# Kernel optimization log

Measured on AMD Instinct MI355X. Metric: run time of the kernel, lower is better.

Reference implementation:

```python
import jax, jax.numpy as jnp
import numpy as np

DIM = 512
CODEBOOK_SIZE = 8192
CODEBOOK_DIM = 13  # log2(8192)
CODEBOOK_SCALE = 1.0
DIVERSITY_GAMMA = 1.0
COMMIT_W = 0.25
ENTROPY_W = 0.1
EPS = 1e-5


def make_codebook():
    mask = 2 ** jnp.arange(CODEBOOK_DIM - 1, -1, -1)  # [13]
    codes = jnp.arange(CODEBOOK_SIZE)
    bits = ((codes[:, None] & mask) != 0).astype(jnp.float32)
    return bits * 2.0 * CODEBOOK_SCALE - CODEBOOK_SCALE  # [8192, 13]


def setup_inputs() -> dict:
    key = jax.random.key(0)
    k1, k2, k3, k4, k5 = jax.random.split(key, 5)
    x = jax.random.normal(k1, (4, 2048, DIM), dtype=jnp.float32)
    w_in = jax.random.normal(k2, (DIM, CODEBOOK_DIM), dtype=jnp.float32) * (DIM ** -0.5)
    b_in = jax.random.normal(k3, (CODEBOOK_DIM,), dtype=jnp.float32) * 0.01
    w_out = jax.random.normal(k4, (CODEBOOK_DIM, DIM), dtype=jnp.float32) * (CODEBOOK_DIM ** -0.5)
    b_out = jax.random.normal(k5, (DIM,), dtype=jnp.float32) * 0.01
    return {"x": x, "w_in": w_in, "b_in": b_in, "w_out": w_out, "b_out": b_out,
            "codebook": make_codebook()}


def reference(x, w_in, b_in, w_out, b_out, codebook):
    # project_in: [b, n, dim] -> [b, n, cd]
    h = jnp.einsum('bnd,dc->bnc', x, w_in) + b_in
    original_input = h

    # sign quantization
    quantized = jnp.where(h > 0, CODEBOOK_SCALE, -CODEBOOK_SCALE).astype(h.dtype)
    bit_mask = 2 ** jnp.arange(CODEBOOK_DIM - 1, -1, -1, dtype=jnp.int32)
    indices = jnp.sum((quantized > 0).astype(jnp.int32) * bit_mask, axis=-1)  # [b, n]

    # straight-through estimator (training branch)
    xq = h + jax.lax.stop_gradient(quantized - h)

    # entropy aux loss: affinity = -distance = 2 * <orig, codebook>
    logits = 2.0 * jnp.einsum('bnc,kc->bnk', original_input, codebook)  # [b, n, K]
    probs = jax.nn.softmax(logits, axis=-1)
    log_probs = jax.nn.log_softmax(logits + EPS, axis=-1)
    per_sample_entropy = -jnp.mean(jnp.sum(probs * log_probs, axis=-1))
    avg_probs = jnp.mean(probs.reshape(-1, CODEBOOK_SIZE), axis=0)
    codebook_entropy = -jnp.sum(avg_probs * jnp.log(avg_probs + EPS))
    entropy_aux_loss = 1.0 * per_sample_entropy - DIVERSITY_GAMMA * codebook_entropy

    # commitment loss
    commit_loss = jnp.mean((original_input - jax.lax.stop_gradient(quantized)) ** 2)

    # project_out
    out = jnp.einsum('bnc,cd->bnd', xq, w_out) + b_out

    aux_loss = entropy_aux_loss * ENTROPY_W + commit_loss * COMMIT_W
    return out, indices, aux_loss
```

## Files before the change

### kernel.cpp

```cpp
#include <hip/hip_runtime.h>
#include <math.h>

#define NTOK 8192
#define DIMV 512
#define CD 13
#define KSZ 8192
#define NPARTS 512
#define TPB 16

#define C_BYTES  ((size_t)NPARTS * KSZ * 4)
#define PC_OFF   C_BYTES
#define E_OFF    (PC_OFF + 4096)
#define CNT_OFF  (E_OFF + 1024)

__global__ __launch_bounds__(512) void ka_fused(const float* __restrict__ x,
                                                const float* __restrict__ w_in,
                                                const float* __restrict__ b_in,
                                                const float* __restrict__ w_out,
                                                const float* __restrict__ b_out,
                                                float* __restrict__ ws_C,
                                                float* __restrict__ ws_pc,
                                                unsigned int* __restrict__ ws_cnt,
                                                float* __restrict__ outv,
                                                float* __restrict__ out_ind) {
  __shared__ __align__(16) float s_winT[CD * DIMV];
  __shared__ float sh[TPB][CD];
  __shared__ __align__(16) float sA[TPB][4][16];
  __shared__ __align__(16) float sB[TPB][128];
  __shared__ float s_cm[TPB], s_pe[TPB];
  int t = threadIdx.x;

  if (blockIdx.x == 0 && t == 0) *ws_cnt = 0u;

  {
    int d = t;
#pragma unroll
    for (int c = 0; c < CD; ++c) s_winT[c * DIMV + d] = w_in[d * CD + c];
  }
  __syncthreads();

  int lane = t & 63;
  int wave = t >> 6;
  int l31 = lane & 31;
  int grp = lane >> 5;
  int tok = wave * 2 + grp;
  int n = blockIdx.x * TPB + tok;

  const float4* x4 = (const float4*)(x + (size_t)n * DIMV);

  float facc[CD];
#pragma unroll
  for (int c = 0; c < CD; ++c) facc[c] = 0.f;
#pragma unroll
  for (int j = 0; j < 4; ++j) {
    float4 xv = x4[l31 + j * 32];
    int dbase = (l31 + j * 32) * 4;
#pragma unroll
    for (int c = 0; c < CD; ++c) {
      const float4 wv = *(const float4*)&s_winT[c * DIMV + dbase];
      facc[c] += xv.x * wv.x + xv.y * wv.y + xv.z * wv.z + xv.w * wv.w;
    }
  }
  double acc[CD];
#pragma unroll
  for (int c = 0; c < CD; ++c) {
    double a = (double)facc[c];
    a += __shfl_xor(a, 1, 64);
    a += __shfl_xor(a, 2, 64);
    a += __shfl_xor(a, 4, 64);
    a += __shfl_xor(a, 8, 64);
    a += __shfl_xor(a, 16, 64);
    acc[c] = a + (double)b_in[c];
  }

  int idx = 0;
#pragma unroll
  for (int c = 0; c < CD; ++c) idx |= (acc[c] > 0.0 ? 1 : 0) << (12 - c);
  if (l31 == 0) out_ind[n] = (float)idx;

  float hv = 0.f;
#pragma unroll
  for (int c = 0; c < CD; ++c) if (l31 == c) hv = (float)acc[c];
  float cm = 0.f, pe = 0.f;
  if (l31 < CD) {
    sh[tok][l31] = hv;
    float a = fabsf(hv);
    float d1 = a - 1.f;
    cm = d1 * d1;
    float z = 4.f * a;
    float e = expf(-z);
    pe = log1pf(e) + z * e / (1.f + e);
  }
  cm += __shfl_xor(cm, 1, 64); pe += __shfl_xor(pe, 1, 64);
  cm += __shfl_xor(cm, 2, 64); pe += __shfl_xor(pe, 2, 64);
  cm += __shfl_xor(cm, 4, 64); pe += __shfl_xor(pe, 4, 64);
  cm += __shfl_xor(cm, 8, 64); pe += __shfl_xor(pe, 8, 64);
  cm += __shfl_xor(cm, 16, 64); pe += __shfl_xor(pe, 16, 64);
  if (l31 == 0) { s_cm[tok] = cm; s_pe[tok] = pe; }

  int dpos = lane * 4;
  int id2[2];
  id2[0] = __shfl(idx, 0, 64);
  id2[1] = __shfl(idx, 32, 64);
  float4 o[2][2];
  {
    float4 bo0 = *(const float4*)(b_out + dpos);
    float4 bo1 = *(const float4*)(b_out + dpos + 256);
#pragma unroll
    for (int tt = 0; tt < 2; ++tt) { o[tt][0] = bo0; o[tt][1] = bo1; }
  }
#pragma unroll
  for (int c = 0; c < CD; ++c) {
    const float4 w0 = *(const float4*)&w_out[c * DIMV + dpos];
    const float4 w1 = *(const float4*)&w_out[c * DIMV + dpos + 256];
#pragma unroll
    for (int tt = 0; tt < 2; ++tt) {
      float sgn = ((id2[tt] >> (12 - c)) & 1) ? 1.f : -1.f;
      o[tt][0].x = fmaf(sgn, w0.x, o[tt][0].x);
      o[tt][0].y = fmaf(sgn, w0.y, o[tt][0].y);
      o[tt][0].z = fmaf(sgn, w0.z, o[tt][0].z);
      o[tt][0].w = fmaf(sgn, w0.w, o[tt][0].w);
      o[tt][1].x = fmaf(sgn, w1.x, o[tt][1].x);
      o[tt][1].y = fmaf(sgn, w1.y, o[tt][1].y);
      o[tt][1].z = fmaf(sgn, w1.z, o[tt][1].z);
      o[tt][1].w = fmaf(sgn, w1.w, o[tt][1].w);
    }
  }
  int n0 = blockIdx.x * TPB + wave * 2;
#pragma unroll
  for (int tt = 0; tt < 2; ++tt) {
    float4* dst = (float4*)(outv + (size_t)(n0 + tt) * DIMV);
    dst[lane] = o[tt][0];
    dst[lane + 64] = o[tt][1];
  }

  __syncthreads();
  if (t == 0) {
    float C = 0.f, P = 0.f;
#pragma unroll
    for (int i = 0; i < TPB; ++i) { C += s_cm[i]; P += s_pe[i]; }
    ws_pc[blockIdx.x * 2] = C;
    ws_pc[blockIdx.x * 2 + 1] = P;
  }

#pragma unroll
  for (int mm = 0; mm < 2; ++mm) {
    int m = wave * 2 + mm;
    float p[CD], q[CD];
#pragma unroll
    for (int c = 0; c < CD; ++c) {
      float hvv = sh[m][c];
      float e = expf(-4.f * hvv);
      float r = 1.f / (1.f + e);
      p[c] = r;
      q[c] = e * r;
    }
    float A = ((lane >> 5) & 1) ? p[0] : q[0];
    A *= ((lane >> 4) & 1) ? p[1] : q[1];
    A *= ((lane >> 3) & 1) ? p[2] : q[2];
    A *= ((lane >> 2) & 1) ? p[3] : q[3];
    A *= ((lane >> 1) & 1) ? p[4] : q[4];
    A *= (lane & 1) ? p[5] : q[5];
    sA[m][lane & 3][lane >> 2] = A;
    float Bb = ((lane >> 5) & 1) ? p[7] : q[7];
    Bb *= ((lane >> 4) & 1) ? p[8] : q[8];
    Bb *= ((lane >> 3) & 1) ? p[9] : q[9];
    Bb *= ((lane >> 2) & 1) ? p[10] : q[10];
    Bb *= ((lane >> 1) & 1) ? p[11] : q[11];
    Bb *= (lane & 1) ? p[12] : q[12];
    sB[m][lane] = q[6] * Bb;
    sB[m][64 + lane] = p[6] * Bb;
  }
  __syncthreads();

  int c2 = t >> 7;
  int klo = t & 127;
  float acc2[16];
#pragma unroll
  for (int j = 0; j < 16; ++j) acc2[j] = 0.f;
  for (int m = 0; m < TPB; ++m) {
    float Bv = sB[m][klo];
    const float4* A4 = (const float4*)&sA[m][c2][0];
#pragma unroll
    for (int jj = 0; jj < 4; ++jj) {
      float4 a = A4[jj];
      acc2[jj * 4 + 0] = fmaf(a.x, Bv, acc2[jj * 4 + 0]);
      acc2[jj * 4 + 1] = fmaf(a.y, Bv, acc2[jj * 4 + 1]);
      acc2[jj * 4 + 2] = fmaf(a.z, Bv, acc2[jj * 4 + 2]);
      acc2[jj * 4 + 3] = fmaf(a.w, Bv, acc2[jj * 4 + 3]);
    }
  }
  float* dst = ws_C + (size_t)blockIdx.x * KSZ;
#pragma unroll
  for (int j = 0; j < 16; ++j) dst[t + 512 * j] = acc2[j];
}

__global__ __launch_bounds__(256) void kb_final(const float* __restrict__ ws_C,
                                                const float* __restrict__ ws_pc,
                                                float* __restrict__ ws_e,
                                                unsigned int* __restrict__ ws_cnt,
                                                float* __restrict__ d_aux) {
  __shared__ float red[256];
  __shared__ int s_last;
  int t = threadIdx.x;
  int sl = t & 31, pg = t >> 5;
  int s = blockIdx.x * 32 + sl;
  float a0 = 0.f, a1 = 0.f, a2 = 0.f, a3 = 0.f;
  for (int i = 0; i < 64; i += 4) {
    a0 += ws_C[(size_t)(pg + 8 * (i + 0)) * KSZ + s];
    a1 += ws_C[(size_t)(pg + 8 * (i + 1)) * KSZ + s];
    a2 += ws_C[(size_t)(pg + 8 * (i + 2)) * KSZ + s];
    a3 += ws_C[(size_t)(pg + 8 * (i + 3)) * KSZ + s];
  }
  red[t] = (a0 + a1) + (a2 + a3);
  __syncthreads();
  float contrib = 0.f;
  if (t < 32) {
    float v = red[t];
#pragma unroll
    for (int j = 1; j < 8; ++j) v += red[t + 32 * j];
    float avg = v * (1.f / (float)NTOK);
    contrib = -avg * logf(avg + 1e-5f);
  }
  if (t < 64) {
    contrib += __shfl_xor(contrib, 1, 64);
    contrib += __shfl_xor(contrib, 2, 64);
    contrib += __shfl_xor(contrib, 4, 64);
    contrib += __shfl_xor(contrib, 8, 64);
    contrib += __shfl_xor(contrib, 16, 64);
    if (t == 0) ws_e[blockIdx.x] = contrib;
  }
  if (t == 0) {
    __threadfence();
    unsigned int old = atomicAdd(ws_cnt, 1u);
    s_last = (old == 255u) ? 1 : 0;
  }
  __syncthreads();
  if (s_last) {
    __threadfence();
    __shared__ float rc[256], rp[256], re[256];
    float cm2 = 0.f, pe2 = 0.f;
    for (int i = t; i < 512; i += 256) {
      cm2 += ws_pc[2 * i];
      pe2 += ws_pc[2 * i + 1];
    }
    rc[t] = cm2; rp[t] = pe2; re[t] = ws_e[t];
    __syncthreads();
    if (t < 64) {
      float C = rc[t] + rc[t + 64] + rc[t + 128] + rc[t + 192];
      float P = rp[t] + rp[t + 64] + rp[t + 128] + rp[t + 192];
      float E = re[t] + re[t + 64] + re[t + 128] + re[t + 192];
      C += __shfl_xor(C, 1, 64); P += __shfl_xor(P, 1, 64); E += __shfl_xor(E, 1, 64);
      C += __shfl_xor(C, 2, 64); P += __shfl_xor(P, 2, 64); E += __shfl_xor(E, 2, 64);
      C += __shfl_xor(C, 4, 64); P += __shfl_xor(P, 4, 64); E += __shfl_xor(E, 4, 64);
      C += __shfl_xor(C, 8, 64); P += __shfl_xor(P, 8, 64); E += __shfl_xor(E, 8, 64);
      C += __shfl_xor(C, 16, 64); P += __shfl_xor(P, 16, 64); E += __shfl_xor(E, 16, 64);
      C += __shfl_xor(C, 32, 64); P += __shfl_xor(P, 32, 64); E += __shfl_xor(E, 32, 64);
      if (t == 0) {
        float commit = C * (1.f / (float)(NTOK * CD));
        float psE = P * (1.f / (float)NTOK);
        d_aux[0] = 0.1f * (psE - E) + 0.25f * commit;
      }
    }
  }
}

extern "C" void kernel_launch(void* const* d_in, const int* in_sizes, int n_in,
                              void* d_out, int out_size, void* d_ws, size_t ws_size,
                              hipStream_t stream) {
  const float* x     = (const float*)d_in[0];
  const float* w_in  = (const float*)d_in[1];
  const float* b_in  = (const float*)d_in[2];
  const float* w_out = (const float*)d_in[3];
  const float* b_out = (const float*)d_in[4];

  float* outv = (float*)d_out;
  float* ind  = outv + (size_t)NTOK * DIMV;
  float* aux  = ind + NTOK;

  float*        ws_C   = (float*)d_ws;
  float*        ws_pc  = (float*)((char*)d_ws + PC_OFF);
  float*        ws_e   = (float*)((char*)d_ws + E_OFF);
  unsigned int* ws_cnt = (unsigned int*)((char*)d_ws + CNT_OFF);

  ka_fused<<<NPARTS, 512, 0, stream>>>(x, w_in, b_in, w_out, b_out,
                                       ws_C, ws_pc, ws_cnt, outv, ind);
  kb_final<<<256, 256, 0, stream>>>(ws_C, ws_pc, ws_e, ws_cnt, aux);
}
```

Measured before the change: 43.22 us.

## Halve block size, read w_in from global, and register-tile the codebook outer product

The fused kernel now runs 256 threads per block instead of 512, so each wave handles four tokens instead of two. The shared-memory transpose of w_in is dropped: each lane loads its 52 w_in values straight from global (L2-cached) into registers. The per-block A⊗B outer product is re-tiled so each thread computes an 8x4 register tile with float4 LDS reads and float4 stores, replacing scalar strided stores. This removes the w_in staging and its barrier and improves store vectorisation, at the cost of more registers per thread and fewer threads per block.

```diff
diff --git a/kernel.cpp b/kernel.cpp
--- a/kernel.cpp
+++ b/kernel.cpp
@@ -13,7 +13,7 @@
 #define E_OFF    (PC_OFF + 4096)
 #define CNT_OFF  (E_OFF + 1024)
 
-__global__ __launch_bounds__(512) void ka_fused(const float* __restrict__ x,
+__global__ __launch_bounds__(256) void ka_fused(const float* __restrict__ x,
                                                 const float* __restrict__ w_in,
                                                 const float* __restrict__ b_in,
                                                 const float* __restrict__ w_out,
@@ -23,118 +23,126 @@
                                                 unsigned int* __restrict__ ws_cnt,
                                                 float* __restrict__ outv,
                                                 float* __restrict__ out_ind) {
-  __shared__ __align__(16) float s_winT[CD * DIMV];
   __shared__ float sh[TPB][CD];
-  __shared__ __align__(16) float sA[TPB][4][16];
+  __shared__ __align__(16) float sA[TPB][64];
   __shared__ __align__(16) float sB[TPB][128];
   __shared__ float s_cm[TPB], s_pe[TPB];
   int t = threadIdx.x;
 
   if (blockIdx.x == 0 && t == 0) *ws_cnt = 0u;
-
-  {
-    int d = t;
-#pragma unroll
-    for (int c = 0; c < CD; ++c) s_winT[c * DIMV + d] = w_in[d * CD + c];
-  }
-  __syncthreads();
 
   int lane = t & 63;
   int wave = t >> 6;
   int l31 = lane & 31;
   int grp = lane >> 5;
-  int tok = wave * 2 + grp;
-  int n = blockIdx.x * TPB + tok;
-
-  const float4* x4 = (const float4*)(x + (size_t)n * DIMV);
-
-  float facc[CD];
-#pragma unroll
-  for (int c = 0; c < CD; ++c) facc[c] = 0.f;
-#pragma unroll
-  for (int j = 0; j < 4; ++j) {
-    float4 xv = x4[l31 + j * 32];
-    int dbase = (l31 + j * 32) * 4;
+  int tok = wave * 4 + grp * 2;
+  const float4* wf4 = (const float4*)w_in;
+
+#pragma unroll
+  for (int tt = 0; tt < 2; ++tt) {
+    int tk = tok + tt;
+    int n = blockIdx.x * TPB + tk;
+    const float4* x4 = (const float4*)(x + (size_t)n * DIMV);
+
+    float facc[CD];
+#pragma unroll
+    for (int c = 0; c < CD; ++c) facc[c] = 0.f;
+#pragma unroll
+    for (int j = 0; j < 4; ++j) {
+      int dbase = (l31 + j * 32) * 4;
+      float4 xv = x4[l31 + j * 32];
+      float wreg[52];
+      const float4* wsrc = wf4 + (size_t)(dbase * CD) / 4;
+#pragma unroll
+      for (int k = 0; k < 13; ++k) *(float4*)&wreg[k * 4] = wsrc[k];
+#pragma unroll
+      for (int c = 0; c < CD; ++c) {
+        facc[c] += xv.x * wreg[c] + xv.y * wreg[13 + c] +
+                   xv.z * wreg[26 + c] + xv.w * wreg[39 + c];
+      }
+    }
+    double acc[CD];
 #pragma unroll
     for (int c = 0; c < CD; ++c) {
-      const float4 wv = *(const float4*)&s_winT[c * DIMV + dbase];
-      facc[c] += xv.x * wv.x + xv.y * wv.y + xv.z * wv.z + xv.w * wv.w;
-    }
-  }
-  double acc[CD];
-#pragma unroll
-  for (int c = 0; c < CD; ++c) {
-    double a = (double)facc[c];
-    a += __shfl_xor(a, 1, 64);
-    a += __shfl_xor(a, 2, 64);
-    a += __shfl_xor(a, 4, 64);
-    a += __shfl_xor(a, 8, 64);
-    a += __shfl_xor(a, 16, 64);
-    acc[c] = a + (double)b_in[c];
-  }
-
-  int idx = 0;
-#pragma unroll
-  for (int c = 0; c < CD; ++c) idx |= (acc[c] > 0.0 ? 1 : 0) << (12 - c);
-  if (l31 == 0) out_ind[n] = (float)idx;
-
-  float hv = 0.f;
-#pragma unroll
-  for (int c = 0; c < CD; ++c) if (l31 == c) hv = (float)acc[c];
-  float cm = 0.f, pe = 0.f;
-  if (l31 < CD) {
-    sh[tok][l31] = hv;
-    float a = fabsf(hv);
-    float d1 = a - 1.f;
-    cm = d1 * d1;
-    float z = 4.f * a;
-    float e = expf(-z);
-    pe = log1pf(e) + z * e / (1.f + e);
-  }
-  cm += __shfl_xor(cm, 1, 64); pe += __shfl_xor(pe, 1, 64);
-  cm += __shfl_xor(cm, 2, 64); pe += __shfl_xor(pe, 2, 64);
-  cm += __shfl_xor(cm, 4, 64); pe += __shfl_xor(pe, 4, 64);
-  cm += __shfl_xor(cm, 8, 64); pe += __shfl_xor(pe, 8, 64);
-  cm += __shfl_xor(cm, 16, 64); pe += __shfl_xor(pe, 16, 64);
-  if (l31 == 0) { s_cm[tok] = cm; s_pe[tok] = pe; }
-
-  int dpos = lane * 4;
-  int id2[2];
-  id2[0] = __shfl(idx, 0, 64);
-  id2[1] = __shfl(idx, 32, 64);
-  float4 o[2][2];
+      double a = (double)facc[c];
+      a += __shfl_xor(a, 1, 64);
+      a += __shfl_xor(a, 2, 64);
+      a += __shfl_xor(a, 4, 64);
+      a += __shfl_xor(a, 8, 64);
+      a += __shfl_xor(a, 16, 64);
+      acc[c] = a + (double)b_in[c];
+    }
+
+    int idx = 0;
+#pragma unroll
+    for (int c = 0; c < CD; ++c) idx |= (acc[c] > 0.0 ? 1 : 0) << (12 - c);
+    if (l31 == 0) out_ind[n] = (float)idx;
+
+    float hv = 0.f;
+#pragma unroll
+    for (int c = 0; c < CD; ++c) if (l31 == c) hv = (float)acc[c];
+    float cm = 0.f, pe = 0.f;
+    if (l31 < CD) {
+      sh[tk][l31] = hv;
+      float a = fabsf(hv);
+      float d1 = a - 1.f;
+      cm = d1 * d1;
+      float z = 4.f * a;
+      float e = expf(-z);
+      pe = log1pf(e) + z * e / (1.f + e);
+    }
+    cm += __shfl_xor(cm, 1, 64); pe += __shfl_xor(pe, 1, 64);
+    cm += __shfl_xor(cm, 2, 64); pe += __shfl_xor(pe, 2, 64);
+    cm += __shfl_xor(cm, 4, 64); pe += __shfl_xor(pe, 4, 64);
+    cm += __shfl_xor(cm, 8, 64); pe += __shfl_xor(pe, 8, 64);
+    cm += __shfl_xor(cm, 16, 64); pe += __shfl_xor(pe, 16, 64);
+    if (l31 == 0) { s_cm[tk] = cm; s_pe[tk] = pe; }
+
+  }
+
+  __syncthreads();
   {
+    int dpos = lane * 4;
     float4 bo0 = *(const float4*)(b_out + dpos);
     float4 bo1 = *(const float4*)(b_out + dpos + 256);
-#pragma unroll
-    for (int tt = 0; tt < 2; ++tt) { o[tt][0] = bo0; o[tt][1] = bo1; }
-  }
-#pragma unroll
-  for (int c = 0; c < CD; ++c) {
-    const float4 w0 = *(const float4*)&w_out[c * DIMV + dpos];
-    const float4 w1 = *(const float4*)&w_out[c * DIMV + dpos + 256];
-#pragma unroll
-    for (int tt = 0; tt < 2; ++tt) {
-      float sgn = ((id2[tt] >> (12 - c)) & 1) ? 1.f : -1.f;
-      o[tt][0].x = fmaf(sgn, w0.x, o[tt][0].x);
-      o[tt][0].y = fmaf(sgn, w0.y, o[tt][0].y);
-      o[tt][0].z = fmaf(sgn, w0.z, o[tt][0].z);
-      o[tt][0].w = fmaf(sgn, w0.w, o[tt][0].w);
-      o[tt][1].x = fmaf(sgn, w1.x, o[tt][1].x);
-      o[tt][1].y = fmaf(sgn, w1.y, o[tt][1].y);
-      o[tt][1].z = fmaf(sgn, w1.z, o[tt][1].z);
-      o[tt][1].w = fmaf(sgn, w1.w, o[tt][1].w);
-    }
-  }
-  int n0 = blockIdx.x * TPB + wave * 2;
-#pragma unroll
-  for (int tt = 0; tt < 2; ++tt) {
-    float4* dst = (float4*)(outv + (size_t)(n0 + tt) * DIMV);
-    dst[lane] = o[tt][0];
-    dst[lane + 64] = o[tt][1];
-  }
-
-  __syncthreads();
+    int base_tok = wave * 4;
+    float4 o[4][2];
+    int id2[4];
+#pragma unroll
+    for (int ttk = 0; ttk < 4; ++ttk) {
+      o[ttk][0] = bo0; o[ttk][1] = bo1;
+      int id = 0;
+#pragma unroll
+      for (int c = 0; c < CD; ++c)
+        id |= (sh[base_tok + ttk][c] > 0.f ? 1 : 0) << (12 - c);
+      id2[ttk] = id;
+    }
+#pragma unroll
+    for (int c = 0; c < CD; ++c) {
+      const float4 w0 = *(const float4*)&w_out[c * DIMV + dpos];
+      const float4 w1 = *(const float4*)&w_out[c * DIMV + dpos + 256];
+#pragma unroll
+      for (int ttk = 0; ttk < 4; ++ttk) {
+        float sgn = ((id2[ttk] >> (12 - c)) & 1) ? 1.f : -1.f;
+        o[ttk][0].x = fmaf(sgn, w0.x, o[ttk][0].x);
+        o[ttk][0].y = fmaf(sgn, w0.y, o[ttk][0].y);
+        o[ttk][0].z = fmaf(sgn, w0.z, o[ttk][0].z);
+        o[ttk][0].w = fmaf(sgn, w0.w, o[ttk][0].w);
+        o[ttk][1].x = fmaf(sgn, w1.x, o[ttk][1].x);
+        o[ttk][1].y = fmaf(sgn, w1.y, o[ttk][1].y);
+        o[ttk][1].z = fmaf(sgn, w1.z, o[ttk][1].z);
+        o[ttk][1].w = fmaf(sgn, w1.w, o[ttk][1].w);
+      }
+    }
+    int n0 = blockIdx.x * TPB + base_tok;
+#pragma unroll
+    for (int ttk = 0; ttk < 4; ++ttk) {
+      float4* dst = (float4*)(outv + (size_t)(n0 + ttk) * DIMV);
+      dst[lane] = o[ttk][0];
+      dst[lane + 64] = o[ttk][1];
+    }
+  }
+
   if (t == 0) {
     float C = 0.f, P = 0.f;
 #pragma unroll
@@ -143,9 +151,7 @@
     ws_pc[blockIdx.x * 2 + 1] = P;
   }
 
-#pragma unroll
-  for (int mm = 0; mm < 2; ++mm) {
-    int m = wave * 2 + mm;
+  for (int m = wave; m < TPB; m += 4) {
     float p[CD], q[CD];
 #pragma unroll
     for (int c = 0; c < CD; ++c) {
@@ -161,7 +167,7 @@
     A *= ((lane >> 2) & 1) ? p[3] : q[3];
     A *= ((lane >> 1) & 1) ? p[4] : q[4];
     A *= (lane & 1) ? p[5] : q[5];
-    sA[m][lane & 3][lane >> 2] = A;
+    sA[m][lane] = A;
     float Bb = ((lane >> 5) & 1) ? p[7] : q[7];
     Bb *= ((lane >> 4) & 1) ? p[8] : q[8];
     Bb *= ((lane >> 3) & 1) ? p[9] : q[9];
@@ -173,26 +179,30 @@
   }
   __syncthreads();
 
-  int c2 = t >> 7;
-  int klo = t & 127;
-  float acc2[16];
-#pragma unroll
-  for (int j = 0; j < 16; ++j) acc2[j] = 0.f;
+  int kh0 = (t >> 5) << 3;
+  int kl0 = (t & 31) << 2;
+  float4 acc4[8];
+#pragma unroll
+  for (int a = 0; a < 8; ++a) acc4[a] = make_float4(0.f, 0.f, 0.f, 0.f);
   for (int m = 0; m < TPB; ++m) {
-    float Bv = sB[m][klo];
-    const float4* A4 = (const float4*)&sA[m][c2][0];
-#pragma unroll
-    for (int jj = 0; jj < 4; ++jj) {
-      float4 a = A4[jj];
-      acc2[jj * 4 + 0] = fmaf(a.x, Bv, acc2[jj * 4 + 0]);
-      acc2[jj * 4 + 1] = fmaf(a.y, Bv, acc2[jj * 4 + 1]);
-      acc2[jj * 4 + 2] = fmaf(a.z, Bv, acc2[jj * 4 + 2]);
-      acc2[jj * 4 + 3] = fmaf(a.w, Bv, acc2[jj * 4 + 3]);
-    }
-  }
-  float* dst = ws_C + (size_t)blockIdx.x * KSZ;
-#pragma unroll
-  for (int j = 0; j < 16; ++j) dst[t + 512 * j] = acc2[j];
+    float4 bv = *(const float4*)&sB[m][kl0];
+    float4 av0 = *(const float4*)&sA[m][kh0];
+    float4 av1 = *(const float4*)&sA[m][kh0 + 4];
+    float Aa[8] = {av0.x, av0.y, av0.z, av0.w, av1.x, av1.y, av1.z, av1.w};
+#pragma unroll
+    for (int a = 0; a < 8; ++a) {
+      acc4[a].x = fmaf(Aa[a], bv.x, acc4[a].x);
+      acc4[a].y = fmaf(Aa[a], bv.y, acc4[a].y);
+      acc4[a].z = fmaf(Aa[a], bv.z, acc4[a].z);
+      acc4[a].w = fmaf(Aa[a], bv.w, acc4[a].w);
+    }
+  }
+  {
+    float* dst = ws_C + (size_t)blockIdx.x * KSZ;
+#pragma unroll
+    for (int a = 0; a < 8; ++a)
+      *(float4*)&dst[(kh0 + a) * 128 + kl0] = acc4[a];
+  }
 }
 
 __global__ __launch_bounds__(256) void kb_final(const float* __restrict__ ws_C,
@@ -283,7 +293,7 @@
   float*        ws_e   = (float*)((char*)d_ws + E_OFF);
   unsigned int* ws_cnt = (unsigned int*)((char*)d_ws + CNT_OFF);
 
-  ka_fused<<<NPARTS, 512, 0, stream>>>(x, w_in, b_in, w_out, b_out,
+  ka_fused<<<NPARTS, 256, 0, stream>>>(x, w_in, b_in, w_out, b_out,
                                        ws_C, ws_pc, ws_cnt, outv, ind);
   kb_final<<<256, 256, 0, stream>>>(ws_C, ws_pc, ws_e, ws_cnt, aux);
 }
```

New measurement: 53.84 us. 24.6% more time.
